# Kernel optimization log

Measured on AMD Instinct MI355X. Metric: run time of the kernel, lower is better.

Reference implementation:

```python
import jax, jax.numpy as jnp
import numpy as np

N_NODES = 100_000
N_EDGES = 3_200_000
N_GRAPHS = 256
F_IN = 128


def setup_inputs() -> dict:
    key = jax.random.key(0)
    ks = jax.random.split(key, 12)
    x = jax.random.normal(ks[0], (N_NODES, F_IN), dtype=jnp.float32)
    edge_weight = jax.random.uniform(ks[1], (N_EDGES,), dtype=jnp.float32)
    W1 = jax.random.normal(ks[2], (F_IN, 16), dtype=jnp.float32) * (1.0 / np.sqrt(F_IN))
    b1 = jnp.zeros((16,), jnp.float32)
    W2 = jax.random.normal(ks[3], (16, 16), dtype=jnp.float32) * 0.25
    b2 = jnp.zeros((16,), jnp.float32)
    Wd2 = jax.random.normal(ks[4], (16, 16), dtype=jnp.float32) * 0.25
    bd2 = jnp.zeros((16,), jnp.float32)
    Wd3 = jax.random.normal(ks[5], (16, 2), dtype=jnp.float32) * 0.25
    bd3 = jnp.zeros((2,), jnp.float32)
    row = jax.random.randint(ks[6], (N_EDGES,), 0, N_NODES, dtype=jnp.int32)
    col = jax.random.randint(ks[7], (N_EDGES,), 0, N_NODES, dtype=jnp.int32)
    seg = jnp.sort(jax.random.randint(ks[8], (N_NODES,), 0, N_GRAPHS, dtype=jnp.int32))
    return {"x": x, "edge_weight": edge_weight, "W1": W1, "b1": b1, "W2": W2,
            "b2": b2, "Wd2": Wd2, "bd2": bd2, "Wd3": Wd3, "bd3": bd3,
            "row": row, "col": col, "seg": seg}


def _gcn_conv(x, row, col, w, kernel, bias):
    # Spektral GCNConv: out = A_norm @ (x @ kernel) + bias
    h = x @ kernel                                   # [N, C]
    msg = h[col] * w[:, None]                        # gather + weight, [E, C]
    agg = jax.ops.segment_sum(msg, row, num_segments=N_NODES)  # scatter-add
    return agg + bias


def reference(x, edge_weight, W1, b1, W2, b2, Wd2, bd2, Wd3, bd3, row, col, seg):
    h = jax.nn.elu(_gcn_conv(x, row, col, edge_weight, W1, b1))
    h = jax.nn.elu(_gcn_conv(h, row, col, edge_weight, W2, b2))
    pooled = jax.ops.segment_sum(h, seg, num_segments=N_GRAPHS)  # [G, 16]
    out = jax.nn.relu(pooled @ Wd2 + bd2)
    # Dropout is identity at inference time
    out = jax.nn.sigmoid(out @ Wd3 + bd3)            # [G, 2]
    return out
```

## Files before the change

kernel.cpp:

```cpp
#include <hip/hip_runtime.h>

#define N_NODES 100000
#define N_EDGES 3200000
#define N_GRAPHS 256

typedef unsigned short bf16_t;

__device__ __forceinline__ bf16_t f2bf(float f) {
    unsigned u = __float_as_uint(f);
    u += 0x7FFFu + ((u >> 16) & 1u);
    return (bf16_t)(u >> 16);
}
__device__ __forceinline__ float bf2f(bf16_t b) {
    return __uint_as_float(((unsigned)b) << 16);
}

__global__ __launch_bounds__(256) void gemm1_kernel(const float* __restrict__ x,
                                                    const float* __restrict__ W1,
                                                    bf16_t* __restrict__ out) {
    __shared__ float w1s[128 * 16];
    const int tid = threadIdx.x;
    {
        const float4* ws = (const float4*)W1;
        float4* wd = (float4*)w1s;
        wd[tid] = ws[tid];
        wd[tid + 256] = ws[tid + 256];
    }
    __syncthreads();
    const int node = blockIdx.x * 256 + tid;
    if (node >= N_NODES) return;
    const float4* xr = (const float4*)(x + (size_t)node * 128);
    float acc[16];
#pragma unroll
    for (int j = 0; j < 16; ++j) acc[j] = 0.f;
#pragma unroll 4
    for (int k4 = 0; k4 < 32; ++k4) {
        const float4 xv = xr[k4];
        const float* wr = &w1s[k4 * 64];
#pragma unroll
        for (int j = 0; j < 16; ++j)
            acc[j] = fmaf(xv.x, wr[j],
                     fmaf(xv.y, wr[16 + j],
                     fmaf(xv.z, wr[32 + j],
                     fmaf(xv.w, wr[48 + j], acc[j]))));
    }
    uint4 p0, p1;
    p0.x = f2bf(acc[0]) | ((unsigned)f2bf(acc[1]) << 16);
    p0.y = f2bf(acc[2]) | ((unsigned)f2bf(acc[3]) << 16);
    p0.z = f2bf(acc[4]) | ((unsigned)f2bf(acc[5]) << 16);
    p0.w = f2bf(acc[6]) | ((unsigned)f2bf(acc[7]) << 16);
    p1.x = f2bf(acc[8]) | ((unsigned)f2bf(acc[9]) << 16);
    p1.y = f2bf(acc[10]) | ((unsigned)f2bf(acc[11]) << 16);
    p1.z = f2bf(acc[12]) | ((unsigned)f2bf(acc[13]) << 16);
    p1.w = f2bf(acc[14]) | ((unsigned)f2bf(acc[15]) << 16);
    uint4* dst = (uint4*)(out + (size_t)node * 16);
    dst[0] = p0;
    dst[1] = p1;
}

__global__ __launch_bounds__(256) void gemm16f_kernel(const float* __restrict__ hraw,
                                                      const float* __restrict__ bias,
                                                      const float* __restrict__ W,
                                                      bf16_t* __restrict__ out) {
    __shared__ float wsm[256];
    __shared__ float bs[16];
    const int tid = threadIdx.x;
    wsm[tid] = W[tid];
    if (tid < 16) bs[tid] = bias[tid];
    __syncthreads();
    const int node = blockIdx.x * 256 + tid;
    if (node >= N_NODES) return;
    const float4* hr = (const float4*)(hraw + (size_t)node * 16);
    float hv[16];
#pragma unroll
    for (int q = 0; q < 4; ++q) {
        const float4 v = hr[q];
        float a0 = v.x + bs[q * 4 + 0], a1 = v.y + bs[q * 4 + 1];
        float a2 = v.z + bs[q * 4 + 2], a3 = v.w + bs[q * 4 + 3];
        hv[q * 4 + 0] = a0 > 0.f ? a0 : expm1f(a0);
        hv[q * 4 + 1] = a1 > 0.f ? a1 : expm1f(a1);
        hv[q * 4 + 2] = a2 > 0.f ? a2 : expm1f(a2);
        hv[q * 4 + 3] = a3 > 0.f ? a3 : expm1f(a3);
    }
    float acc[16];
#pragma unroll
    for (int j = 0; j < 16; ++j) acc[j] = 0.f;
#pragma unroll
    for (int k = 0; k < 16; ++k) {
#pragma unroll
        for (int j = 0; j < 16; ++j)
            acc[j] = fmaf(hv[k], wsm[k * 16 + j], acc[j]);
    }
    uint4 p0, p1;
    p0.x = f2bf(acc[0]) | ((unsigned)f2bf(acc[1]) << 16);
    p0.y = f2bf(acc[2]) | ((unsigned)f2bf(acc[3]) << 16);
    p0.z = f2bf(acc[4]) | ((unsigned)f2bf(acc[5]) << 16);
    p0.w = f2bf(acc[6]) | ((unsigned)f2bf(acc[7]) << 16);
    p1.x = f2bf(acc[8]) | ((unsigned)f2bf(acc[9]) << 16);
    p1.y = f2bf(acc[10]) | ((unsigned)f2bf(acc[11]) << 16);
    p1.z = f2bf(acc[12]) | ((unsigned)f2bf(acc[13]) << 16);
    p1.w = f2bf(acc[14]) | ((unsigned)f2bf(acc[15]) << 16);
    uint4* dst = (uint4*)(out + (size_t)node * 16);
    dst[0] = p0;
    dst[1] = p1;
}

__global__ __launch_bounds__(256) void scatter_kernel(const bf16_t* __restrict__ h,
                                                      const float* __restrict__ w,
                                                      const int* __restrict__ row,
                                                      const int* __restrict__ col,
                                                      float* __restrict__ agg) {
    const long long t = (long long)blockIdx.x * 256 + threadIdx.x;
    const int e = (int)(t >> 4);
    const int ch = (int)(t & 15);
    const int r = row[e], c = col[e];
    const float wt = w[e];
    const float hv = bf2f(h[(size_t)c * 16 + ch]);
    atomicAdd(agg + (size_t)r * 16 + ch, hv * wt);
}

#define POOL_NODES 128
__global__ __launch_bounds__(256) void poolf_kernel(const float* __restrict__ hraw,
                                                    const float* __restrict__ bias,
                                                    const int* __restrict__ seg,
                                                    float* __restrict__ pooled) {
    __shared__ float lp[N_GRAPHS * 16];
    __shared__ float bs[16];
    const int tid = threadIdx.x;
    if (tid < 16) bs[tid] = bias[tid];
    for (int i = tid; i < N_GRAPHS * 16; i += 256) lp[i] = 0.f;
    __syncthreads();
    const int base = blockIdx.x * POOL_NODES;
    const int lim = min(base + POOL_NODES, N_NODES);
    const int nf4 = (lim - base) * 4;
    const float4* src = (const float4*)(hraw + (size_t)base * 16);
    for (int i = tid; i < nf4; i += 256) {
        const float4 v = src[i];
        const int node = base + (i >> 2);
        const int ch0 = (i & 3) * 4;
        float* d = &lp[seg[node] * 16 + ch0];
        float a0 = v.x + bs[ch0 + 0], a1 = v.y + bs[ch0 + 1];
        float a2 = v.z + bs[ch0 + 2], a3 = v.w + bs[ch0 + 3];
        atomicAdd(d + 0, a0 > 0.f ? a0 : expm1f(a0));
        atomicAdd(d + 1, a1 > 0.f ? a1 : expm1f(a1));
        atomicAdd(d + 2, a2 > 0.f ? a2 : expm1f(a2));
        atomicAdd(d + 3, a3 > 0.f ? a3 : expm1f(a3));
    }
    __syncthreads();
    const int s0 = seg[base];
    const int s1 = seg[lim - 1];
    const int cnt = (s1 - s0 + 1) * 16;
    for (int j = tid; j < cnt; j += 256) {
        atomicAdd(&pooled[s0 * 16 + j], lp[s0 * 16 + j]);
    }
}

__global__ __launch_bounds__(256) void head_kernel(const float* __restrict__ pooled,
                                                   const float* __restrict__ Wd2,
                                                   const float* __restrict__ bd2,
                                                   const float* __restrict__ Wd3,
                                                   const float* __restrict__ bd3,
                                                   float* __restrict__ out) {
    __shared__ float w2[256], w3[32], b2s[16], b3s[2];
    const int tid = threadIdx.x;
    w2[tid] = Wd2[tid];
    if (tid < 32) w3[tid] = Wd3[tid];
    if (tid < 16) b2s[tid] = bd2[tid];
    if (tid < 2) b3s[tid] = bd3[tid];
    __syncthreads();
    const int g = tid;
    float p[16];
#pragma unroll
    for (int k = 0; k < 16; ++k) p[k] = pooled[g * 16 + k];
    float t[16];
#pragma unroll
    for (int j = 0; j < 16; ++j) {
        float acc = b2s[j];
#pragma unroll
        for (int k = 0; k < 16; ++k) acc = fmaf(p[k], w2[k * 16 + j], acc);
        t[j] = acc > 0.f ? acc : 0.f;
    }
#pragma unroll
    for (int m = 0; m < 2; ++m) {
        float acc = b3s[m];
#pragma unroll
        for (int j = 0; j < 16; ++j) acc = fmaf(t[j], w3[j * 2 + m], acc);
        out[g * 2 + m] = 1.f / (1.f + expf(-acc));
    }
}

extern "C" void kernel_launch(void* const* d_in, const int* in_sizes, int n_in,
                              void* d_out, int out_size, void* d_ws, size_t ws_size,
                              hipStream_t stream) {
    const float* x   = (const float*)d_in[0];
    const float* ew  = (const float*)d_in[1];
    const float* W1  = (const float*)d_in[2];
    const float* b1  = (const float*)d_in[3];
    const float* W2  = (const float*)d_in[4];
    const float* b2  = (const float*)d_in[5];
    const float* Wd2 = (const float*)d_in[6];
    const float* bd2 = (const float*)d_in[7];
    const float* Wd3 = (const float*)d_in[8];
    const float* bd3 = (const float*)d_in[9];
    const int* row   = (const int*)d_in[10];
    const int* col   = (const int*)d_in[11];
    const int* seg   = (const int*)d_in[12];
    float* out = (float*)d_out;

    char* wsc = (char*)d_ws;
    bf16_t* A    = (bf16_t*)wsc;
    float*  B    = (float*)(wsc + 3200000);
    float* pooled= (float*)(wsc + 9600000);

    const size_t h_bytes = (size_t)N_NODES * 16 * sizeof(float);
    const int scatter_blocks = (int)(((long long)N_EDGES * 16) / 256);
    const int node_blocks = (N_NODES + 255) / 256;

    gemm1_kernel<<<node_blocks, 256, 0, stream>>>(x, W1, A);
    hipMemsetAsync(B, 0, h_bytes, stream);
    scatter_kernel<<<scatter_blocks, 256, 0, stream>>>(A, ew, row, col, B);

    gemm16f_kernel<<<node_blocks, 256, 0, stream>>>(B, b1, W2, A);
    hipMemsetAsync(B, 0, h_bytes, stream);
    scatter_kernel<<<scatter_blocks, 256, 0, stream>>>(A, ew, row, col, B);

    hipMemsetAsync(pooled, 0, N_GRAPHS * 16 * sizeof(float), stream);
    poolf_kernel<<<(N_NODES + POOL_NODES - 1) / POOL_NODES, 256, 0, stream>>>(B, b2, seg, pooled);
    head_kernel<<<1, 256, 0, stream>>>(pooled, Wd2, bd2, Wd3, bd3, out);
}
```

Before: 507.2 us.

## Fold buffer zeroing into GEMM kernels and store features in fp32

Removes the three hipMemsetAsync calls. Each GEMM kernel now zeroes the aggregation buffer in place after reading it (or writes zeros alongside its output), and block 0 of the second GEMM clears the pooled accumulator. The per-node feature buffer feeding the scatter is also changed from bf16 to fp32, so the conversion code goes away. In exchange, the scatter's random gathers read twice as many bytes, and the feature buffer takes more memory.

```diff
diff --git a/kernel.cpp b/kernel.cpp
--- a/kernel.cpp
+++ b/kernel.cpp
@@ -4,20 +4,10 @@
 #define N_EDGES 3200000
 #define N_GRAPHS 256
 
-typedef unsigned short bf16_t;
-
-__device__ __forceinline__ bf16_t f2bf(float f) {
-    unsigned u = __float_as_uint(f);
-    u += 0x7FFFu + ((u >> 16) & 1u);
-    return (bf16_t)(u >> 16);
-}
-__device__ __forceinline__ float bf2f(bf16_t b) {
-    return __uint_as_float(((unsigned)b) << 16);
-}
-
 __global__ __launch_bounds__(256) void gemm1_kernel(const float* __restrict__ x,
                                                     const float* __restrict__ W1,
-                                                    bf16_t* __restrict__ out) {
+                                                    float* __restrict__ outA,
+                                                    float* __restrict__ zeroB) {
     __shared__ float w1s[128 * 16];
     const int tid = threadIdx.x;
     {
@@ -44,33 +34,36 @@
                      fmaf(xv.z, wr[32 + j],
                      fmaf(xv.w, wr[48 + j], acc[j]))));
     }
-    uint4 p0, p1;
-    p0.x = f2bf(acc[0]) | ((unsigned)f2bf(acc[1]) << 16);
-    p0.y = f2bf(acc[2]) | ((unsigned)f2bf(acc[3]) << 16);
-    p0.z = f2bf(acc[4]) | ((unsigned)f2bf(acc[5]) << 16);
-    p0.w = f2bf(acc[6]) | ((unsigned)f2bf(acc[7]) << 16);
-    p1.x = f2bf(acc[8]) | ((unsigned)f2bf(acc[9]) << 16);
-    p1.y = f2bf(acc[10]) | ((unsigned)f2bf(acc[11]) << 16);
-    p1.z = f2bf(acc[12]) | ((unsigned)f2bf(acc[13]) << 16);
-    p1.w = f2bf(acc[14]) | ((unsigned)f2bf(acc[15]) << 16);
-    uint4* dst = (uint4*)(out + (size_t)node * 16);
-    dst[0] = p0;
-    dst[1] = p1;
-}
-
-__global__ __launch_bounds__(256) void gemm16f_kernel(const float* __restrict__ hraw,
+    float4* dst = (float4*)(outA + (size_t)node * 16);
+#pragma unroll
+    for (int q = 0; q < 4; ++q)
+        dst[q] = make_float4(acc[q * 4], acc[q * 4 + 1], acc[q * 4 + 2], acc[q * 4 + 3]);
+    float4* bz = (float4*)(zeroB + (size_t)node * 16);
+    const float4 z = make_float4(0.f, 0.f, 0.f, 0.f);
+#pragma unroll
+    for (int q = 0; q < 4; ++q) bz[q] = z;
+}
+
+__global__ __launch_bounds__(256) void gemm16f_kernel(float* __restrict__ Braw,
                                                       const float* __restrict__ bias,
                                                       const float* __restrict__ W,
-                                                      bf16_t* __restrict__ out) {
+                                                      float* __restrict__ outA,
+                                                      float* __restrict__ pooled) {
     __shared__ float wsm[256];
     __shared__ float bs[16];
     const int tid = threadIdx.x;
     wsm[tid] = W[tid];
     if (tid < 16) bs[tid] = bias[tid];
+    if (blockIdx.x == 0) {
+        float4* pz = (float4*)pooled;
+        const float4 z = make_float4(0.f, 0.f, 0.f, 0.f);
+#pragma unroll
+        for (int q = 0; q < 4; ++q) pz[tid * 4 + q] = z;
+    }
     __syncthreads();
     const int node = blockIdx.x * 256 + tid;
     if (node >= N_NODES) return;
-    const float4* hr = (const float4*)(hraw + (size_t)node * 16);
+    float4* hr = (float4*)(Braw + (size_t)node * 16);
     float hv[16];
 #pragma unroll
     for (int q = 0; q < 4; ++q) {
@@ -91,21 +84,16 @@
         for (int j = 0; j < 16; ++j)
             acc[j] = fmaf(hv[k], wsm[k * 16 + j], acc[j]);
     }
-    uint4 p0, p1;
-    p0.x = f2bf(acc[0]) | ((unsigned)f2bf(acc[1]) << 16);
-    p0.y = f2bf(acc[2]) | ((unsigned)f2bf(acc[3]) << 16);
-    p0.z = f2bf(acc[4]) | ((unsigned)f2bf(acc[5]) << 16);
-    p0.w = f2bf(acc[6]) | ((unsigned)f2bf(acc[7]) << 16);
-    p1.x = f2bf(acc[8]) | ((unsigned)f2bf(acc[9]) << 16);
-    p1.y = f2bf(acc[10]) | ((unsigned)f2bf(acc[11]) << 16);
-    p1.z = f2bf(acc[12]) | ((unsigned)f2bf(acc[13]) << 16);
-    p1.w = f2bf(acc[14]) | ((unsigned)f2bf(acc[15]) << 16);
-    uint4* dst = (uint4*)(out + (size_t)node * 16);
-    dst[0] = p0;
-    dst[1] = p1;
-}
-
-__global__ __launch_bounds__(256) void scatter_kernel(const bf16_t* __restrict__ h,
+    float4* dst = (float4*)(outA + (size_t)node * 16);
+#pragma unroll
+    for (int q = 0; q < 4; ++q)
+        dst[q] = make_float4(acc[q * 4], acc[q * 4 + 1], acc[q * 4 + 2], acc[q * 4 + 3]);
+    const float4 z = make_float4(0.f, 0.f, 0.f, 0.f);
+#pragma unroll
+    for (int q = 0; q < 4; ++q) hr[q] = z;
+}
+
+__global__ __launch_bounds__(256) void scatter_kernel(const float* __restrict__ h,
                                                       const float* __restrict__ w,
                                                       const int* __restrict__ row,
                                                       const int* __restrict__ col,
@@ -115,8 +103,7 @@
     const int ch = (int)(t & 15);
     const int r = row[e], c = col[e];
     const float wt = w[e];
-    const float hv = bf2f(h[(size_t)c * 16 + ch]);
-    atomicAdd(agg + (size_t)r * 16 + ch, hv * wt);
+    atomicAdd(agg + (size_t)r * 16 + ch, h[(size_t)c * 16 + ch] * wt);
 }
 
 #define POOL_NODES 128
@@ -207,24 +194,19 @@
     const int* seg   = (const int*)d_in[12];
     float* out = (float*)d_out;
 
-    char* wsc = (char*)d_ws;
-    bf16_t* A    = (bf16_t*)wsc;
-    float*  B    = (float*)(wsc + 3200000);
-    float* pooled= (float*)(wsc + 9600000);
-
-    const size_t h_bytes = (size_t)N_NODES * 16 * sizeof(float);
+    float* A = (float*)d_ws;
+    float* B = A + (size_t)N_NODES * 16;
+    float* pooled = B + (size_t)N_NODES * 16;
+
     const int scatter_blocks = (int)(((long long)N_EDGES * 16) / 256);
     const int node_blocks = (N_NODES + 255) / 256;
 
-    gemm1_kernel<<<node_blocks, 256, 0, stream>>>(x, W1, A);
-    hipMemsetAsync(B, 0, h_bytes, stream);
+    gemm1_kernel<<<node_blocks, 256, 0, stream>>>(x, W1, A, B);
     scatter_kernel<<<scatter_blocks, 256, 0, stream>>>(A, ew, row, col, B);
 
-    gemm16f_kernel<<<node_blocks, 256, 0, stream>>>(B, b1, W2, A);
-    hipMemsetAsync(B, 0, h_bytes, stream);
+    gemm16f_kernel<<<node_blocks, 256, 0, stream>>>(B, b1, W2, A, pooled);
     scatter_kernel<<<scatter_blocks, 256, 0, stream>>>(A, ew, row, col, B);
 
-    hipMemsetAsync(pooled, 0, N_GRAPHS * 16 * sizeof(float), stream);
     poolf_kernel<<<(N_NODES + POOL_NODES - 1) / POOL_NODES, 256, 0, stream>>>(B, b2, seg, pooled);
     head_kernel<<<1, 256, 0, stream>>>(pooled, Wd2, bd2, Wd3, bd3, out);
 }
```

Measured after the change: 497.0 us. -2.0%, faster.
